# Kernel optimization log

Hardware: AMD Instinct MI355X
Metric: run time of the kernel (lower is better)

The kernel has to match this reference:

```python
import jax, jax.numpy as jnp
import numpy as np

CHUNK = 128


def selective_scan(x, A, Bm, Cm, dt, chunk_size):
    # x: [B,L,H,hd], Bm/Cm: [B,L,H,ds], A/dt: [H]. L must be divisible by chunk_size.
    Bb, L, H, hd = x.shape
    ds = Bm.shape[-1]
    cs = chunk_size
    nc = L // cs
    decay = jnp.exp(A * dt)  # [H]
    x_c = x.reshape(Bb, nc, cs, H, hd).transpose(0, 1, 3, 2, 4)   # [B,nc,H,cs,hd]
    B_c = Bm.reshape(Bb, nc, cs, H, ds).transpose(0, 1, 3, 2, 4)  # [B,nc,H,cs,ds]
    C_c = Cm.reshape(Bb, nc, cs, H, ds).transpose(0, 1, 3, 2, 4)
    x_dt = x_c * dt[None, None, :, None, None]
    idx = jnp.arange(cs, dtype=x.dtype)
    diff = idx[:, None] - idx[None, :]
    # causal intra-chunk decay matrix [H,cs,cs]
    L_mat = jnp.where(diff >= 0, decay[:, None, None] ** jnp.maximum(diff, 0.0), 0.0)
    CB = jnp.einsum('bnhid,bnhjd->bnhij', C_c, B_c)          # [B,nc,H,cs,cs]
    y_diag = jnp.einsum('bnhij,bnhjd->bnhid', CB * L_mat[None, None], x_dt)
    rev = jnp.arange(cs - 1, -1, -1, dtype=x.dtype)
    decay_rev = decay[:, None] ** rev[None, :]               # [H,cs]
    B_w = B_c * decay_rev[None, None, :, :, None]
    states = jnp.einsum('bnhjs,bnhjd->bnhsd', B_w, x_dt)     # [B,nc,H,ds,hd]
    cidx = jnp.arange(nc, dtype=x.dtype)
    shift = cidx[:, None] - cidx[None, :] - 1.0
    chunk_decay = decay ** cs
    M = jnp.where(shift >= 0, chunk_decay[:, None, None] ** jnp.maximum(shift, 0.0), 0.0)  # [H,nc,nc]
    h_carry = jnp.einsum('hij,bjhsd->bihsd', M, states)      # [B,nc,H,ds,hd]
    decay_out = decay[:, None] ** (idx[None, :] + 1.0)       # [H,cs]
    y_off = jnp.einsum('bnhis,bnhsd->bnhid', C_c, h_carry) * decay_out[None, None, :, :, None]
    y = (y_diag + y_off).transpose(0, 1, 3, 2, 4).reshape(Bb, L, H, hd)
    return y


def setup_inputs() -> dict:
    key = jax.random.key(0)
    ks = jax.random.split(key, 9)
    B, L, d_model, d_inner, H, ds, K = 2, 4096, 1024, 2048, 16, 128, 4
    s_dm = 1.0 / np.sqrt(d_model)
    s_di = 1.0 / np.sqrt(d_inner)
    x = jax.random.normal(ks[0], (B, L, d_model), jnp.float32)
    x_prenorm = jax.random.normal(ks[1], (B, L, d_model), jnp.float32)
    in_proj_w = jax.random.normal(ks[2], (2 * d_inner, d_model), jnp.float32) * s_dm
    conv_w = jax.random.normal(ks[3], (d_inner, 1, K), jnp.float32) * 0.5
    conv_b = jax.random.normal(ks[4], (d_inner,), jnp.float32) * 0.01
    B_proj_w = jax.random.normal(ks[5], (H * ds, d_model), jnp.float32) * s_dm
    C_proj_w = jax.random.normal(ks[6], (H * ds, d_model), jnp.float32) * s_dm
    dt_init = jax.random.uniform(ks[7], (H,), jnp.float32, 0.001, 0.1)
    dt_bias = dt_init + jnp.log(-jnp.expm1(-dt_init))  # inverse softplus
    A_log = jnp.log(jnp.arange(1, H + 1, dtype=jnp.float32))
    D_param = jnp.ones((H,), jnp.float32)
    out_proj_w = jax.random.normal(ks[8], (d_model, d_inner), jnp.float32) * s_di
    return dict(x=x, x_prenorm=x_prenorm, in_proj_w=in_proj_w, conv_w=conv_w,
                conv_b=conv_b, B_proj_w=B_proj_w, C_proj_w=C_proj_w,
                dt_bias=dt_bias, A_log=A_log, D_param=D_param, out_proj_w=out_proj_w)


def reference(x, x_prenorm, in_proj_w, conv_w, conv_b, B_proj_w, C_proj_w,
              dt_bias, A_log, D_param, out_proj_w):
    Bb, L, d_model = x.shape
    H = A_log.shape[0]
    ds = B_proj_w.shape[0] // H
    vg = x @ in_proj_w.T                        # [B,L,2*d_inner]
    d_inner = vg.shape[-1] // 2
    value, gate = vg[..., :d_inner], vg[..., d_inner:]
    K = conv_w.shape[-1]
    # causal depthwise conv1d (torch pads K-1 both sides then truncates right)
    v = jax.lax.conv_general_dilated(
        value.transpose(0, 2, 1), conv_w, (1,), [(K - 1, 0)],
        feature_group_count=d_inner, dimension_numbers=('NCH', 'OIH', 'NCH'))
    v = v + conv_b[None, :, None]
    value = jax.nn.silu(v.transpose(0, 2, 1))   # [B,L,d_inner]
    Bm = (x_prenorm @ B_proj_w.T).reshape(Bb, L, H, ds)
    Cm = (x_prenorm @ C_proj_w.T).reshape(Bb, L, H, ds)
    dt = jax.nn.softplus(dt_bias)
    A = -jnp.exp(A_log)
    hd = d_inner // H
    vh = value.reshape(Bb, L, H, hd)
    y = selective_scan(vh, A, Bm, Cm, dt, CHUNK)
    y = y + D_param[None, None, :, None] * vh
    y = y.reshape(Bb, L, d_inner) * jax.nn.silu(gate)
    return y @ out_proj_w.T
```

## Files before the change

### kernel.cpp

```cpp
#include <hip/hip_runtime.h>
#include <hip/hip_bf16.h>

#define NB 2
#define LSEQ 4096
#define DM 1024
#define DI 2048
#define NH 16
#define DSZ 128
#define CS 128
#define NCHUNK 32

using bf16 = __hip_bfloat16;
typedef __attribute__((ext_vector_type(8))) short short8;
typedef __attribute__((ext_vector_type(4))) float f32x4;

__device__ __forceinline__ float b2f(unsigned short u) {
    union { unsigned i; float f; } c; c.i = ((unsigned)u) << 16; return c.f;
}
__device__ __forceinline__ bf16 f2bf(float v) { return __float2bfloat16(v); }
__device__ __forceinline__ float bf2f(bf16 v) { return __bfloat162float(v); }

__device__ __forceinline__ float head_dt(const float* dt_bias, int h) {
    return log1pf(expf(dt_bias[h]));
}
__device__ __forceinline__ float head_l2dec(const float* dt_bias, const float* A_log, int h, float* dt_out) {
    float dt = head_dt(dt_bias, h);
    *dt_out = dt;
    return -expf(A_log[h]) * dt * 1.4426950408889634f;
}

__device__ __forceinline__ void storeC(bf16* C, size_t idx, float v) { C[idx] = f2bf(v); }
__device__ __forceinline__ void storeC(float* C, size_t idx, float v) { C[idx] = v; }

__device__ __forceinline__ void gload16(const bf16* g, bf16* l) {
    __builtin_amdgcn_global_load_lds(
        (const __attribute__((address_space(1))) void*)g,
        (__attribute__((address_space(3))) void*)l, 16, 0, 0);
}

__global__ __launch_bounds__(256) void cast_f2b(const float* __restrict__ in,
                                                bf16* __restrict__ out, long n) {
    long i = ((long)blockIdx.x * 256 + threadIdx.x) * 8;
    if (i >= n) return;
    float4 a = *reinterpret_cast<const float4*>(in + i);
    float4 b = *reinterpret_cast<const float4*>(in + i + 4);
    union { bf16 h[8]; short8 v; } o;
    o.h[0] = f2bf(a.x); o.h[1] = f2bf(a.y); o.h[2] = f2bf(a.z); o.h[3] = f2bf(a.w);
    o.h[4] = f2bf(b.x); o.h[5] = f2bf(b.y); o.h[6] = f2bf(b.z); o.h[7] = f2bf(b.w);
    *reinterpret_cast<short8*>(out + i) = o.v;
}

template <int MODE, typename TO>
__global__ __launch_bounds__(256) void gemm_mfma(const bf16* __restrict__ A,
                                                 const bf16* __restrict__ W,
                                                 TO* __restrict__ C0, TO* __restrict__ C1,
                                                 int N, int K) {
    __shared__ bf16 As[2][128 * 32];
    __shared__ bf16 Ws[2][128 * 32];
    const int tid = threadIdx.x;
    const int lane = tid & 63, w = tid >> 6;
    const int wr = w >> 1, wc = w & 1;
    const int bm = blockIdx.y * 128, bn = blockIdx.x * 128;
    const int srow = lane >> 2;
    const int skoff = (((lane & 3) ^ ((lane >> 2) & 3)) * 8);
    const int g0 = w * 2, g1 = w * 2 + 1;
    const int fr = lane & 15;
    const int fk = (((lane >> 4) ^ (lane & 3)) * 8);
    f32x4 acc[4][4] = {};
#define STAGE(buf, kt)                                                                  \
    do {                                                                                \
        gload16(A + (size_t)(bm + g0 * 16 + srow) * K + (kt) + skoff, &As[buf][g0 * 512]); \
        gload16(A + (size_t)(bm + g1 * 16 + srow) * K + (kt) + skoff, &As[buf][g1 * 512]); \
        gload16(W + (size_t)(bn + g0 * 16 + srow) * K + (kt) + skoff, &Ws[buf][g0 * 512]); \
        gload16(W + (size_t)(bn + g1 * 16 + srow) * K + (kt) + skoff, &Ws[buf][g1 * 512]); \
    } while (0)
    STAGE(0, 0);
    __syncthreads();
    const int NT = K / 32;
    int cur = 0;
    for (int t = 0; t < NT; ++t) {
        if (t + 1 < NT) STAGE(cur ^ 1, (t + 1) * 32);
        short8 af[4], bfr[4];
#pragma unroll
        for (int mi = 0; mi < 4; ++mi)
            af[mi] = *reinterpret_cast<const short8*>(&As[cur][(wr * 64 + mi * 16 + fr) * 32 + fk]);
#pragma unroll
        for (int ni = 0; ni < 4; ++ni)
            bfr[ni] = *reinterpret_cast<const short8*>(&Ws[cur][(wc * 64 + ni * 16 + fr) * 32 + fk]);
#pragma unroll
        for (int mi = 0; mi < 4; ++mi)
#pragma unroll
            for (int ni = 0; ni < 4; ++ni)
                acc[mi][ni] = __builtin_amdgcn_mfma_f32_16x16x32_bf16(af[mi], bfr[ni], acc[mi][ni], 0, 0, 0);
        __syncthreads();
        cur ^= 1;
    }
#undef STAGE
    const int orow0 = (lane >> 4) * 4;
    const int ocol = lane & 15;
#pragma unroll
    for (int mi = 0; mi < 4; ++mi)
#pragma unroll
        for (int ni = 0; ni < 4; ++ni) {
            int col = bn + wc * 64 + ni * 16 + ocol;
#pragma unroll
            for (int r = 0; r < 4; ++r) {
                int row = bm + wr * 64 + mi * 16 + orow0 + r;
                float v = acc[mi][ni][r];
                if (MODE == 1) {
                    if (col < DI) storeC(C0, (size_t)row * DI + col, v);
                    else          storeC(C1, (size_t)row * DI + (col - DI), v);
                } else {
                    storeC(C0, (size_t)row * N + col, v);
                }
            }
        }
}

__global__ __launch_bounds__(256) void conv_xdt(const bf16* __restrict__ vpre,
                                                const float* __restrict__ cw,
                                                const float* __restrict__ cb,
                                                const float* __restrict__ dt_bias,
                                                bf16* __restrict__ XDT) {
    __shared__ bf16 Ts[131][136];
    __shared__ bf16 T2[128][136];
    __shared__ float wks[128][4];
    __shared__ float cbs[128];
    const int tid = threadIdx.x;
    const int bid = blockIdx.x;
    const int h = bid & 15, g = bid >> 4;
    const int n31 = g & 31;
    const float dt = head_dt(dt_bias, h);
    if (tid < 128) {
        float4 w4 = *reinterpret_cast<const float4*>(cw + (h * 128 + tid) * 4);
        wks[tid][0] = w4.x; wks[tid][1] = w4.y; wks[tid][2] = w4.z; wks[tid][3] = w4.w;
        cbs[tid] = cb[h * 128 + tid];
    }
    {
        const int lr = tid >> 4, c8 = (tid & 15) * 8;
        for (int i0 = 0; i0 < 144; i0 += 16) {
            int i = i0 + lr;
            if (i < 131) {
                short8 v = {0, 0, 0, 0, 0, 0, 0, 0};
                if (!(n31 == 0 && i < 3))
                    v = *reinterpret_cast<const short8*>(vpre + (size_t)(g * 128 - 3 + i) * 2048 + h * 128 + c8);
                *reinterpret_cast<short8*>(&Ts[i][c8]) = v;
            }
        }
    }
    __syncthreads();
    {
        const int jr = tid >> 4, d8 = (tid & 15) * 8;
        for (int j0 = 0; j0 < 128; j0 += 16) {
            int j = j0 + jr;
            union { bf16 hh[8]; short8 v; } o;
#pragma unroll
            for (int e = 0; e < 8; ++e) {
                int d = d8 + e;
                float s = cbs[d];
#pragma unroll
                for (int k = 0; k < 4; ++k) s += wks[d][k] * bf2f(Ts[j + k][d]);
                float sil = s / (1.f + expf(-s));
                o.hh[e] = f2bf(sil * dt);
            }
            *reinterpret_cast<short8*>(&T2[j][d8]) = o.v;
        }
    }
    __syncthreads();
    {
        const size_t ob = (size_t)bid * 16384;
        const int d = tid & 127;
        for (int jg = (tid >> 7); jg < 16; jg += 2) {
            int j0 = jg * 8;
            union { bf16 hh[8]; short8 v; } o;
#pragma unroll
            for (int e = 0; e < 8; ++e) o.hh[e] = T2[j0 + e][d];
            *reinterpret_cast<short8*>(XDT + ob + (size_t)d * 128 + j0) = o.v;
        }
    }
}

__global__ __launch_bounds__(256) void transpose_bt(const bf16* __restrict__ in, bf16* __restrict__ outp,
                                                    const float* __restrict__ dt_bias,
                                                    const float* __restrict__ A_log) {
    __shared__ bf16 Ts[128][136];
    __shared__ float dpow[128];
    const int tid = threadIdx.x;
    const int bid = blockIdx.x;
    const int h = bid & 15, bn = bid >> 4;
    float dt; float l2d = head_l2dec(dt_bias, A_log, h, &dt);
    if (tid < 128) dpow[tid] = exp2f((float)(127 - tid) * l2d);
    const size_t base = (size_t)bn * CS * 2048 + (size_t)h * 128;
    {
        const int jr = tid >> 4, c8 = (tid & 15) * 8;
        for (int j0 = 0; j0 < 128; j0 += 16)
            *reinterpret_cast<short8*>(&Ts[j0 + jr][c8]) =
                *reinterpret_cast<const short8*>(in + base + (size_t)(j0 + jr) * 2048 + c8);
    }
    __syncthreads();
    const size_t ob = (size_t)bid * 16384;
    const int d = tid & 127;
    for (int jg = (tid >> 7); jg < 16; jg += 2) {
        int j0 = jg * 8;
        union { bf16 h8[8]; short8 v; } o;
#pragma unroll
        for (int e = 0; e < 8; ++e) o.h8[e] = f2bf(bf2f(Ts[j0 + e][d]) * dpow[j0 + e]);
        *reinterpret_cast<short8*>(outp + ob + (size_t)d * 128 + j0) = o.v;
    }
}

__global__ __launch_bounds__(256) void chunk_statesT(const bf16* __restrict__ XDT,
                                                     const bf16* BTg,
                                                     bf16* STT) {
    __shared__ bf16 XTs[128][72];
    __shared__ bf16 BTs[128][72];
    const int tid = threadIdx.x;
    const size_t ob = (size_t)blockIdx.x * 16384;
    const int lane = tid & 63, w = tid >> 6;
    const int fr = lane & 15, fk = (lane >> 4) * 8;
    f32x4 acc[2][8] = {};
    for (int j0 = 0; j0 < 128; j0 += 64) {
        for (int rr = 0; rr < 128; rr += 32) {
            int row = rr + (tid >> 3);
            int col = (tid & 7) * 8;
            *reinterpret_cast<short8*>(&XTs[row][col]) =
                *reinterpret_cast<const short8*>(XDT + ob + (size_t)row * 128 + j0 + col);
            *reinterpret_cast<short8*>(&BTs[row][col]) =
                *reinterpret_cast<const short8*>(BTg + ob + (size_t)row * 128 + j0 + col);
        }
        __syncthreads();
#pragma unroll
        for (int ks = 0; ks < 2; ++ks) {
            short8 a[2], bfr[8];
#pragma unroll
            for (int mi = 0; mi < 2; ++mi)
                a[mi] = *reinterpret_cast<const short8*>(&XTs[w * 32 + mi * 16 + fr][ks * 32 + fk]);
#pragma unroll
            for (int ni = 0; ni < 8; ++ni)
                bfr[ni] = *reinterpret_cast<const short8*>(&BTs[ni * 16 + fr][ks * 32 + fk]);
#pragma unroll
            for (int mi = 0; mi < 2; ++mi)
#pragma unroll
                for (int ni = 0; ni < 8; ++ni)
                    acc[mi][ni] = __builtin_amdgcn_mfma_f32_16x16x32_bf16(a[mi], bfr[ni], acc[mi][ni], 0, 0, 0);
        }
        __syncthreads();
    }
    const int orow0 = (lane >> 4) * 4, ocol = lane & 15;
#pragma unroll
    for (int mi = 0; mi < 2; ++mi)
#pragma unroll
        for (int ni = 0; ni < 8; ++ni) {
            int s = ni * 16 + ocol;
#pragma unroll
            for (int r = 0; r < 4; ++r) {
                int d = w * 32 + mi * 16 + orow0 + r;
                STT[ob + (size_t)d * 128 + s] = f2bf(acc[mi][ni][r]);
            }
        }
}

__global__ __launch_bounds__(256) void scan_kernel(bf16* __restrict__ ST,
                                                   const float* __restrict__ dt_bias,
                                                   const float* __restrict__ A_log) {
    const int q = blockIdx.x & 7;
    const int h = (blockIdx.x >> 3) & 15;
    const int b = blockIdx.x >> 7;
    float dt; float l2d = head_l2dec(dt_bias, A_log, h, &dt);
    float cd = exp2f(128.f * l2d);
    const int tid = threadIdx.x;
    float r[8] = {};
    for (int n = 0; n < NCHUNK; ++n) {
        size_t base = ((size_t)((b * NCHUNK + n) * NH + h)) * 16384 + (size_t)q * 2048;
#pragma unroll
        for (int e = 0; e < 8; ++e) {
            size_t idx = base + e * 256 + tid;
            float v = bf2f(ST[idx]);
            ST[idx] = f2bf(r[e]);
            r[e] = cd * r[e] + v;
        }
    }
}

__global__ __launch_bounds__(256) void chunk_cbl_y(const bf16* __restrict__ Bm, const bf16* __restrict__ Cm,
                                                   const bf16* __restrict__ STT, const bf16* __restrict__ XDT,
                                                   const float* __restrict__ dt_bias,
                                                   const float* __restrict__ A_log,
                                                   const float* __restrict__ D_param,
                                                   bf16* __restrict__ gateY) {
    __shared__ char smem[36864];
    bf16 (*T1)[72]  = reinterpret_cast<bf16(*)[72]>(smem);
    bf16 (*Bst)[72] = reinterpret_cast<bf16(*)[72]>(smem + 18432);
    bf16 (*Ps)[136] = reinterpret_cast<bf16(*)[136]>(smem);
    const int tid = threadIdx.x;
    const int bid = blockIdx.x;
    const int h = bid & 15, g = bid >> 4;
    float dt; float l2d = head_l2dec(dt_bias, A_log, h, &dt);
    const size_t base = (size_t)g * CS * 2048 + (size_t)h * 128;
    const size_t ob = (size_t)bid * 16384;
    const int lane = tid & 63, w = tid >> 6;
    const int fr = lane & 15, fk = (lane >> 4) * 8;
    const int orow0 = (lane >> 4) * 4, ocol = lane & 15;
    const int strow = tid >> 3, stcol = (tid & 7) * 8;
    f32x4 pacc[2][8] = {};
    for (int s0 = 0; s0 < 128; s0 += 64) {
        for (int rr = 0; rr < 128; rr += 32) {
            int row = rr + strow;
            *reinterpret_cast<short8*>(&T1[row][stcol]) =
                *reinterpret_cast<const short8*>(Cm + base + (size_t)row * 2048 + s0 + stcol);
            *reinterpret_cast<short8*>(&Bst[row][stcol]) =
                *reinterpret_cast<const short8*>(Bm + base + (size_t)row * 2048 + s0 + stcol);
        }
        __syncthreads();
#pragma unroll
        for (int ks = 0; ks < 2; ++ks) {
            short8 a[2], bfr[8];
#pragma unroll
            for (int mi = 0; mi < 2; ++mi)
                a[mi] = *reinterpret_cast<const short8*>(&T1[w * 32 + mi * 16 + fr][ks * 32 + fk]);
#pragma unroll
            for (int ni = 0; ni < 8; ++ni)
                bfr[ni] = *reinterpret_cast<const short8*>(&Bst[ni * 16 + fr][ks * 32 + fk]);
#pragma unroll
            for (int mi = 0; mi < 2; ++mi)
#pragma unroll
                for (int ni = 0; ni < 8; ++ni)
                    pacc[mi][ni] = __builtin_amdgcn_mfma_f32_16x16x32_bf16(a[mi], bfr[ni], pacc[mi][ni], 0, 0, 0);
        }
        __syncthreads();
    }
#pragma unroll
    for (int mi = 0; mi < 2; ++mi)
#pragma unroll
        for (int ni = 0; ni < 8; ++ni) {
            int j = ni * 16 + ocol;
#pragma unroll
            for (int r = 0; r < 4; ++r) {
                int i = w * 32 + mi * 16 + orow0 + r;
                float v = (i >= j) ? pacc[mi][ni][r] * exp2f((float)(i - j) * l2d) : 0.f;
                Ps[i][j] = f2bf(v);
            }
        }
    f32x4 acc[2][8] = {};
#pragma unroll
    for (int ks = 0; ks < 4; ++ks) {
        short8 a[2], bfr[8];
#pragma unroll
        for (int mi = 0; mi < 2; ++mi)
            a[mi] = *reinterpret_cast<const short8*>(Cm + base + (size_t)(w * 32 + mi * 16 + fr) * 2048 + ks * 32 + fk);
#pragma unroll
        for (int ni = 0; ni < 8; ++ni)
            bfr[ni] = *reinterpret_cast<const short8*>(STT + ob + (size_t)(ni * 16 + fr) * 128 + ks * 32 + fk);
#pragma unroll
        for (int mi = 0; mi < 2; ++mi)
#pragma unroll
            for (int ni = 0; ni < 8; ++ni)
                acc[mi][ni] = __builtin_amdgcn_mfma_f32_16x16x32_bf16(a[mi], bfr[ni], acc[mi][ni], 0, 0, 0);
    }
#pragma unroll
    for (int mi = 0; mi < 2; ++mi)
#pragma unroll
        for (int r = 0; r < 4; ++r) {
            int i = w * 32 + mi * 16 + orow0 + r;
            float sc = exp2f((float)(i + 1) * l2d);
#pragma unroll
            for (int ni = 0; ni < 8; ++ni) acc[mi][ni][r] *= sc;
        }
    __syncthreads();
#pragma unroll
    for (int ks = 0; ks < 4; ++ks) {
        short8 a[2], bfr[8];
#pragma unroll
        for (int mi = 0; mi < 2; ++mi)
            a[mi] = *reinterpret_cast<const short8*>(&Ps[w * 32 + mi * 16 + fr][ks * 32 + fk]);
#pragma unroll
        for (int ni = 0; ni < 8; ++ni)
            bfr[ni] = *reinterpret_cast<const short8*>(XDT + ob + (size_t)(ni * 16 + fr) * 128 + ks * 32 + fk);
#pragma unroll
        for (int mi = 0; mi < 2; ++mi)
#pragma unroll
            for (int ni = 0; ni < 8; ++ni)
                acc[mi][ni] = __builtin_amdgcn_mfma_f32_16x16x32_bf16(a[mi], bfr[ni], acc[mi][ni], 0, 0, 0);
    }
    const float Dv = D_param[h];
    const float inv_dt = 1.f / dt;
#pragma unroll
    for (int mi = 0; mi < 2; ++mi)
#pragma unroll
        for (int ni = 0; ni < 8; ++ni) {
            int d = ni * 16 + ocol;
#pragma unroll
            for (int r = 0; r < 4; ++r) {
                int i = w * 32 + mi * 16 + orow0 + r;
                size_t idx = base + (size_t)i * 2048 + d;
                float v = bf2f(XDT[ob + (size_t)d * 128 + i]) * inv_dt;
                float yv = acc[mi][ni][r] + Dv * v;
                float gq = bf2f(gateY[idx]);
                gateY[idx] = f2bf(yv * gq / (1.f + expf(-gq)));
            }
        }
}

extern "C" void kernel_launch(void* const* d_in, const int* in_sizes, int n_in,
                              void* d_out, int out_size, void* d_ws, size_t ws_size,
                              hipStream_t stream) {
    (void)out_size;
    static const int exp_sizes[11] = {
        NB * LSEQ * DM, NB * LSEQ * DM, 2 * DI * DM, DI * 4, DI,
        NH * DSZ * DM, NH * DSZ * DM, NH, NH, NH, DM * DI
    };
    if (n_in != 11) return;
    for (int i = 0; i < 11; ++i) if (in_sizes[i] != exp_sizes[i]) return;

    const float* x         = (const float*)d_in[0];
    const float* x_prenorm = (const float*)d_in[1];
    const float* in_proj_w = (const float*)d_in[2];
    const float* conv_w    = (const float*)d_in[3];
    const float* conv_b    = (const float*)d_in[4];
    const float* B_proj_w  = (const float*)d_in[5];
    const float* C_proj_w  = (const float*)d_in[6];
    const float* dt_bias   = (const float*)d_in[7];
    const float* A_log     = (const float*)d_in[8];
    const float* D_param   = (const float*)d_in[9];
    const float* out_proj_w= (const float*)d_in[10];
    float* out = (float*)d_out;

    const size_t NE = (size_t)NB * LSEQ * DI;
    const size_t SLOT = NE * 2;
    if (ws_size < 5 * SLOT) return;
    char* ws = (char*)d_ws;
    bf16* S0 = (bf16*)(ws);
    bf16* S1 = (bf16*)(ws + SLOT);
    bf16* S2 = (bf16*)(ws + 2 * SLOT);
    bf16* S3 = (bf16*)(ws + 3 * SLOT);
    bf16* S4 = (bf16*)(ws + 4 * SLOT);

    bf16* xb   = (bf16*)d_out;
    bf16* wBCb = (bf16*)((char*)d_out + 16777216);

    const int M = NB * LSEQ;
    const int NC = NB * NCHUNK * NH;
    dim3 blk(256);

    cast_f2b<<<dim3(4096), blk, 0, stream>>>(x, xb, (long)NB * LSEQ * DM);
    cast_f2b<<<dim3(2048), blk, 0, stream>>>(in_proj_w, S3, (long)2 * DI * DM);
    gemm_mfma<1, bf16><<<dim3(2 * DI / 128, M / 128), blk, 0, stream>>>(xb, S3, S0, S1, 2 * DI, DM);
    conv_xdt<<<dim3(NC), blk, 0, stream>>>(S0, conv_w, conv_b, dt_bias, S2);
    cast_f2b<<<dim3(4096), blk, 0, stream>>>(x_prenorm, xb, (long)NB * LSEQ * DM);
    cast_f2b<<<dim3(1024), blk, 0, stream>>>(B_proj_w, wBCb, (long)NH * DSZ * DM);
    cast_f2b<<<dim3(1024), blk, 0, stream>>>(C_proj_w, wBCb + (size_t)NH * DSZ * DM, (long)NH * DSZ * DM);
    gemm_mfma<1, bf16><<<dim3(2 * DI / 128, M / 128), blk, 0, stream>>>(xb, wBCb, S3, S4, 2 * DI, DM);
    transpose_bt<<<dim3(NC), blk, 0, stream>>>(S3, S0, dt_bias, A_log);
    chunk_statesT<<<dim3(NC), blk, 0, stream>>>(S2, S0, S0);
    scan_kernel<<<dim3(NB * NH * 8), blk, 0, stream>>>(S0, dt_bias, A_log);
    chunk_cbl_y<<<dim3(NC), blk, 0, stream>>>(S3, S4, S0, S2, dt_bias, A_log, D_param, S1);
    cast_f2b<<<dim3(1024), blk, 0, stream>>>(out_proj_w, S3, (long)DM * DI);
    gemm_mfma<2, float><<<dim3(DM / 128, M / 128), blk, 0, stream>>>(S1, S3, out, nullptr, DM, DI);
}
```

Before: 408.6 us.

## Use 512 threads in chunk_cbl_y with per-warp 16-row tiles and LUT decays

The chunk output kernel now launches 512 threads (8 waves), so each wave owns 16 output rows instead of 32. This halves per-thread accumulator registers and raises parallelism per block. The intra-chunk and output decay factors are precomputed once into shared-memory tables instead of calling exp2f per element. The two GEMMs (C·h_carry and P·xdt) are interleaved in one loop with separate accumulators. A barrier is added before Ps is read. The cost is more waves per block competing for shared memory and load bandwidth, and the kernel is only part of the total pipeline.

```diff
diff --git a/kernel.cpp b/kernel.cpp
--- a/kernel.cpp
+++ b/kernel.cpp
@@ -282,13 +282,15 @@
     }
 }
 
-__global__ __launch_bounds__(256) void chunk_cbl_y(const bf16* __restrict__ Bm, const bf16* __restrict__ Cm,
+__global__ __launch_bounds__(512) void chunk_cbl_y(const bf16* __restrict__ Bm, const bf16* __restrict__ Cm,
                                                    const bf16* __restrict__ STT, const bf16* __restrict__ XDT,
                                                    const float* __restrict__ dt_bias,
                                                    const float* __restrict__ A_log,
                                                    const float* __restrict__ D_param,
                                                    bf16* __restrict__ gateY) {
     __shared__ char smem[36864];
+    __shared__ float dpw[128];
+    __shared__ float dout[128];
     bf16 (*T1)[72]  = reinterpret_cast<bf16(*)[72]>(smem);
     bf16 (*Bst)[72] = reinterpret_cast<bf16(*)[72]>(smem + 18432);
     bf16 (*Ps)[136] = reinterpret_cast<bf16(*)[136]>(smem);
@@ -299,12 +301,15 @@
     const size_t base = (size_t)g * CS * 2048 + (size_t)h * 128;
     const size_t ob = (size_t)bid * 16384;
     const int lane = tid & 63, w = tid >> 6;
+    const int w16 = w * 16;
     const int fr = lane & 15, fk = (lane >> 4) * 8;
     const int orow0 = (lane >> 4) * 4, ocol = lane & 15;
     const int strow = tid >> 3, stcol = (tid & 7) * 8;
-    f32x4 pacc[2][8] = {};
+    if (tid < 128) dpw[tid] = exp2f((float)tid * l2d);
+    else if (tid < 256) dout[tid - 128] = exp2f((float)(tid - 127) * l2d);
+    f32x4 pacc[8] = {};
     for (int s0 = 0; s0 < 128; s0 += 64) {
-        for (int rr = 0; rr < 128; rr += 32) {
+        for (int rr = 0; rr < 128; rr += 64) {
             int row = rr + strow;
             *reinterpret_cast<short8*>(&T1[row][stcol]) =
                 *reinterpret_cast<const short8*>(Cm + base + (size_t)row * 2048 + s0 + stcol);
@@ -314,91 +319,61 @@
         __syncthreads();
 #pragma unroll
         for (int ks = 0; ks < 2; ++ks) {
-            short8 a[2], bfr[8];
-#pragma unroll
-            for (int mi = 0; mi < 2; ++mi)
-                a[mi] = *reinterpret_cast<const short8*>(&T1[w * 32 + mi * 16 + fr][ks * 32 + fk]);
+            short8 a = *reinterpret_cast<const short8*>(&T1[w16 + fr][ks * 32 + fk]);
+            short8 bfr[8];
 #pragma unroll
             for (int ni = 0; ni < 8; ++ni)
                 bfr[ni] = *reinterpret_cast<const short8*>(&Bst[ni * 16 + fr][ks * 32 + fk]);
 #pragma unroll
-            for (int mi = 0; mi < 2; ++mi)
-#pragma unroll
-                for (int ni = 0; ni < 8; ++ni)
-                    pacc[mi][ni] = __builtin_amdgcn_mfma_f32_16x16x32_bf16(a[mi], bfr[ni], pacc[mi][ni], 0, 0, 0);
+            for (int ni = 0; ni < 8; ++ni)
+                pacc[ni] = __builtin_amdgcn_mfma_f32_16x16x32_bf16(a, bfr[ni], pacc[ni], 0, 0, 0);
         }
         __syncthreads();
     }
 #pragma unroll
-    for (int mi = 0; mi < 2; ++mi)
+    for (int ni = 0; ni < 8; ++ni) {
+        int j = ni * 16 + ocol;
+#pragma unroll
+        for (int r = 0; r < 4; ++r) {
+            int i = w16 + orow0 + r;
+            float v = (i >= j) ? pacc[ni][r] * dpw[i - j] : 0.f;
+            Ps[i][j] = f2bf(v);
+        }
+    }
+    __syncthreads();
+    f32x4 acc1[8] = {}, acc2[8] = {};
+#pragma unroll
+    for (int ks = 0; ks < 4; ++ks) {
+        short8 a1 = *reinterpret_cast<const short8*>(Cm + base + (size_t)(w16 + fr) * 2048 + ks * 32 + fk);
+        short8 a2 = *reinterpret_cast<const short8*>(&Ps[w16 + fr][ks * 32 + fk]);
+        short8 b1[8], b2[8];
+#pragma unroll
+        for (int ni = 0; ni < 8; ++ni)
+            b1[ni] = *reinterpret_cast<const short8*>(STT + ob + (size_t)(ni * 16 + fr) * 128 + ks * 32 + fk);
+#pragma unroll
+        for (int ni = 0; ni < 8; ++ni)
+            b2[ni] = *reinterpret_cast<const short8*>(XDT + ob + (size_t)(ni * 16 + fr) * 128 + ks * 32 + fk);
 #pragma unroll
         for (int ni = 0; ni < 8; ++ni) {
-            int j = ni * 16 + ocol;
-#pragma unroll
-            for (int r = 0; r < 4; ++r) {
-                int i = w * 32 + mi * 16 + orow0 + r;
-                float v = (i >= j) ? pacc[mi][ni][r] * exp2f((float)(i - j) * l2d) : 0.f;
-                Ps[i][j] = f2bf(v);
-            }
-        }
-    f32x4 acc[2][8] = {};
-#pragma unroll
-    for (int ks = 0; ks < 4; ++ks) {
-        short8 a[2], bfr[8];
-#pragma unroll
-        for (int mi = 0; mi < 2; ++mi)
-            a[mi] = *reinterpret_cast<const short8*>(Cm + base + (size_t)(w * 32 + mi * 16 + fr) * 2048 + ks * 32 + fk);
-#pragma unroll
-        for (int ni = 0; ni < 8; ++ni)
-            bfr[ni] = *reinterpret_cast<const short8*>(STT + ob + (size_t)(ni * 16 + fr) * 128 + ks * 32 + fk);
-#pragma unroll
-        for (int mi = 0; mi < 2; ++mi)
-#pragma unroll
-            for (int ni = 0; ni < 8; ++ni)
-                acc[mi][ni] = __builtin_amdgcn_mfma_f32_16x16x32_bf16(a[mi], bfr[ni], acc[mi][ni], 0, 0, 0);
-    }
-#pragma unroll
-    for (int mi = 0; mi < 2; ++mi)
-#pragma unroll
-        for (int r = 0; r < 4; ++r) {
-            int i = w * 32 + mi * 16 + orow0 + r;
-            float sc = exp2f((float)(i + 1) * l2d);
-#pragma unroll
-            for (int ni = 0; ni < 8; ++ni) acc[mi][ni][r] *= sc;
-        }
-    __syncthreads();
-#pragma unroll
-    for (int ks = 0; ks < 4; ++ks) {
-        short8 a[2], bfr[8];
-#pragma unroll
-        for (int mi = 0; mi < 2; ++mi)
-            a[mi] = *reinterpret_cast<const short8*>(&Ps[w * 32 + mi * 16 + fr][ks * 32 + fk]);
-#pragma unroll
-        for (int ni = 0; ni < 8; ++ni)
-            bfr[ni] = *reinterpret_cast<const short8*>(XDT + ob + (size_t)(ni * 16 + fr) * 128 + ks * 32 + fk);
-#pragma unroll
-        for (int mi = 0; mi < 2; ++mi)
-#pragma unroll
-            for (int ni = 0; ni < 8; ++ni)
-                acc[mi][ni] = __builtin_amdgcn_mfma_f32_16x16x32_bf16(a[mi], bfr[ni], acc[mi][ni], 0, 0, 0);
+            acc1[ni] = __builtin_amdgcn_mfma_f32_16x16x32_bf16(a1, b1[ni], acc1[ni], 0, 0, 0);
+            acc2[ni] = __builtin_amdgcn_mfma_f32_16x16x32_bf16(a2, b2[ni], acc2[ni], 0, 0, 0);
+        }
     }
     const float Dv = D_param[h];
     const float inv_dt = 1.f / dt;
 #pragma unroll
-    for (int mi = 0; mi < 2; ++mi)
-#pragma unroll
-        for (int ni = 0; ni < 8; ++ni) {
-            int d = ni * 16 + ocol;
-#pragma unroll
-            for (int r = 0; r < 4; ++r) {
-                int i = w * 32 + mi * 16 + orow0 + r;
-                size_t idx = base + (size_t)i * 2048 + d;
-                float v = bf2f(XDT[ob + (size_t)d * 128 + i]) * inv_dt;
-                float yv = acc[mi][ni][r] + Dv * v;
-                float gq = bf2f(gateY[idx]);
-                gateY[idx] = f2bf(yv * gq / (1.f + expf(-gq)));
-            }
-        }
+    for (int ni = 0; ni < 8; ++ni) {
+        int d = ni * 16 + ocol;
+#pragma unroll
+        for (int r = 0; r < 4; ++r) {
+            int i = w16 + orow0 + r;
+            size_t idx = base + (size_t)i * 2048 + d;
+            float v = bf2f(XDT[ob + (size_t)d * 128 + i]) * inv_dt;
+            float yv = acc1[ni][r] * dout[i] + acc2[ni][r] + Dv * v;
+            float gq = bf2f(gateY[idx]);
+            gateY[idx] = f2bf(yv * gq / (1.f + expf(-gq)));
+        }
+    }
 }
 
 extern "C" void kernel_launch(void* const* d_in, const int* in_sizes, int n_in,
@@ -453,7 +428,7 @@
     transpose_bt<<<dim3(NC), blk, 0, stream>>>(S3, S0, dt_bias, A_log);
     chunk_statesT<<<dim3(NC), blk, 0, stream>>>(S2, S0, S0);
     scan_kernel<<<dim3(NB * NH * 8), blk, 0, stream>>>(S0, dt_bias, A_log);
-    chunk_cbl_y<<<dim3(NC), blk, 0, stream>>>(S3, S4, S0, S2, dt_bias, A_log, D_param, S1);
+    chunk_cbl_y<<<dim3(NC), dim3(512), 0, stream>>>(S3, S4, S0, S2, dt_bias, A_log, D_param, S1);
     cast_f2b<<<dim3(1024), blk, 0, stream>>>(out_proj_w, S3, (long)DM * DI);
     gemm_mfma<2, float><<<dim3(DM / 128, M / 128), blk, 0, stream>>>(S1, S3, out, nullptr, DM, DI);
 }
```

Result: slower. 440.0 us (+7.7%).

## Stage STT/XDT operands in LDS for chunk_cbl_y and swizzle GEMM block order

Applied to the files above, without the earlier changes.

In chunk_cbl_y, the off-diagonal (C·state) and diagonal (P·XDT) matmuls now load their B-operands cooperatively into shared memory in 64-wide halves instead of each wave reading them directly from global memory with strided short8 loads. Ps gets its own region so it survives the T1 staging, which enlarges shared memory from 36 KB to 52 KB. The GEMM kernel also remaps block indices with an 8-way interleave, likely to group tiles that share operands for better L2 reuse across XCDs. The cost is extra barriers and larger LDS use, which may lower occupancy.

```diff
diff --git a/kernel.cpp b/kernel.cpp
--- a/kernel.cpp
+++ b/kernel.cpp
@@ -60,7 +60,11 @@
     const int tid = threadIdx.x;
     const int lane = tid & 63, w = tid >> 6;
     const int wr = w >> 1, wc = w & 1;
-    const int bm = blockIdx.y * 128, bn = blockIdx.x * 128;
+    const unsigned nwgx = gridDim.x;
+    const unsigned id = blockIdx.y * nwgx + blockIdx.x;
+    const unsigned cpx = (nwgx * gridDim.y) >> 3;
+    const unsigned sw = (id & 7) * cpx + (id >> 3);
+    const int bm = (int)(sw / nwgx) * 128, bn = (int)(sw % nwgx) * 128;
     const int srow = lane >> 2;
     const int skoff = (((lane & 3) ^ ((lane >> 2) & 3)) * 8);
     const int g0 = w * 2, g1 = w * 2 + 1;
@@ -288,10 +292,10 @@
                                                    const float* __restrict__ A_log,
                                                    const float* __restrict__ D_param,
                                                    bf16* __restrict__ gateY) {
-    __shared__ char smem[36864];
+    __shared__ char smem[53248];
     bf16 (*T1)[72]  = reinterpret_cast<bf16(*)[72]>(smem);
+    bf16 (*Ps)[136] = reinterpret_cast<bf16(*)[136]>(smem + 18432);
     bf16 (*Bst)[72] = reinterpret_cast<bf16(*)[72]>(smem + 18432);
-    bf16 (*Ps)[136] = reinterpret_cast<bf16(*)[136]>(smem);
     const int tid = threadIdx.x;
     const int bid = blockIdx.x;
     const int h = bid & 15, g = bid >> 4;
@@ -342,20 +346,29 @@
             }
         }
     f32x4 acc[2][8] = {};
-#pragma unroll
-    for (int ks = 0; ks < 4; ++ks) {
-        short8 a[2], bfr[8];
-#pragma unroll
-        for (int mi = 0; mi < 2; ++mi)
-            a[mi] = *reinterpret_cast<const short8*>(Cm + base + (size_t)(w * 32 + mi * 16 + fr) * 2048 + ks * 32 + fk);
-#pragma unroll
-        for (int ni = 0; ni < 8; ++ni)
-            bfr[ni] = *reinterpret_cast<const short8*>(STT + ob + (size_t)(ni * 16 + fr) * 128 + ks * 32 + fk);
-#pragma unroll
-        for (int mi = 0; mi < 2; ++mi)
+    for (int hk = 0; hk < 2; ++hk) {
+        for (int rr = 0; rr < 128; rr += 32) {
+            int row = rr + strow;
+            *reinterpret_cast<short8*>(&T1[row][stcol]) =
+                *reinterpret_cast<const short8*>(STT + ob + (size_t)row * 128 + hk * 64 + stcol);
+        }
+        __syncthreads();
+#pragma unroll
+        for (int ks = 0; ks < 2; ++ks) {
+            short8 a[2], bfr[8];
+#pragma unroll
+            for (int mi = 0; mi < 2; ++mi)
+                a[mi] = *reinterpret_cast<const short8*>(Cm + base + (size_t)(w * 32 + mi * 16 + fr) * 2048 + hk * 64 + ks * 32 + fk);
 #pragma unroll
             for (int ni = 0; ni < 8; ++ni)
-                acc[mi][ni] = __builtin_amdgcn_mfma_f32_16x16x32_bf16(a[mi], bfr[ni], acc[mi][ni], 0, 0, 0);
+                bfr[ni] = *reinterpret_cast<const short8*>(&T1[ni * 16 + fr][ks * 32 + fk]);
+#pragma unroll
+            for (int mi = 0; mi < 2; ++mi)
+#pragma unroll
+                for (int ni = 0; ni < 8; ++ni)
+                    acc[mi][ni] = __builtin_amdgcn_mfma_f32_16x16x32_bf16(a[mi], bfr[ni], acc[mi][ni], 0, 0, 0);
+        }
+        __syncthreads();
     }
 #pragma unroll
     for (int mi = 0; mi < 2; ++mi)
@@ -366,21 +379,29 @@
 #pragma unroll
             for (int ni = 0; ni < 8; ++ni) acc[mi][ni][r] *= sc;
         }
-    __syncthreads();
-#pragma unroll
-    for (int ks = 0; ks < 4; ++ks) {
-        short8 a[2], bfr[8];
-#pragma unroll
-        for (int mi = 0; mi < 2; ++mi)
-            a[mi] = *reinterpret_cast<const short8*>(&Ps[w * 32 + mi * 16 + fr][ks * 32 + fk]);
-#pragma unroll
-        for (int ni = 0; ni < 8; ++ni)
-            bfr[ni] = *reinterpret_cast<const short8*>(XDT + ob + (size_t)(ni * 16 + fr) * 128 + ks * 32 + fk);
-#pragma unroll
-        for (int mi = 0; mi < 2; ++mi)
+    for (int j0 = 0; j0 < 128; j0 += 64) {
+        for (int rr = 0; rr < 128; rr += 32) {
+            int row = rr + strow;
+            *reinterpret_cast<short8*>(&T1[row][stcol]) =
+                *reinterpret_cast<const short8*>(XDT + ob + (size_t)row * 128 + j0 + stcol);
+        }
+        __syncthreads();
+#pragma unroll
+        for (int ks = 0; ks < 2; ++ks) {
+            short8 a[2], bfr[8];
+#pragma unroll
+            for (int mi = 0; mi < 2; ++mi)
+                a[mi] = *reinterpret_cast<const short8*>(&Ps[w * 32 + mi * 16 + fr][j0 + ks * 32 + fk]);
 #pragma unroll
             for (int ni = 0; ni < 8; ++ni)
-                acc[mi][ni] = __builtin_amdgcn_mfma_f32_16x16x32_bf16(a[mi], bfr[ni], acc[mi][ni], 0, 0, 0);
+                bfr[ni] = *reinterpret_cast<const short8*>(&T1[ni * 16 + fr][ks * 32 + fk]);
+#pragma unroll
+            for (int mi = 0; mi < 2; ++mi)
+#pragma unroll
+                for (int ni = 0; ni < 8; ++ni)
+                    acc[mi][ni] = __builtin_amdgcn_mfma_f32_16x16x32_bf16(a[mi], bfr[ni], acc[mi][ni], 0, 0, 0);
+        }
+        __syncthreads();
     }
     const float Dv = D_param[h];
     const float inv_dt = 1.f / dt;
```

New measurement: 396.9 us. 1.03x faster.
